# Performance work log

Hardware: AMD Instinct MI355X
Metric: run time of the kernel (lower is better)

Reference implementation:

```python
import jax, jax.numpy as jnp
import numpy as np

B, C, K, F = 16, 64, 128, 6
HORIZON_S = 3.0  # conflict_horizon_s default
EPS = 1e-06


def setup_inputs() -> dict:
    rng = np.random.default_rng(0)
    # base adjacency: sparse random directed graph, zero diagonal
    A = (rng.random((B, K, K)) < 0.05).astype(np.float32)
    A[:, np.arange(K), np.arange(K)] = 0.0
    # candidates: exactly one unordered-pair edit (state in {0:none,1:i->j,2:j->i})
    cand = np.repeat(A[:, None], C, axis=1).copy()
    i = rng.integers(0, K - 1, (B, C))
    j = i + 1 + (rng.integers(0, K - 1, (B, C)) % (K - 1 - i))
    state = rng.integers(0, 3, (B, C))
    bidx = np.arange(B)[:, None] * np.ones((1, C), dtype=np.int64)
    cidx = np.ones((B, 1), dtype=np.int64) * np.arange(C)[None, :]
    cand[bidx, cidx, i, j] = (state == 1).astype(np.float32)
    cand[bidx, cidx, j, i] = (state == 2).astype(np.float32)
    cand[:, 0] = A  # candidate 0 is NOOP (keep A_t)
    # agent features: (x, y, yaw, vx, vy, pad)
    feat = rng.normal(size=(B, K, F)).astype(np.float32)
    feat[..., 0:2] *= 20.0  # spread positions over ~40m
    mask = (rng.random((B, K)) > 0.1).astype(np.float32)
    return {
        "A_t": jnp.asarray(A),
        "candidate_A": jnp.asarray(cand),
        "agent_feat": jnp.asarray(feat),
        "agent_mask": jnp.asarray(mask),
    }


def _edit_tokens(A_t, candidate_A):
    # vectorized version of EBSTM.extract_edit_tokens
    Bn, Cn, Kn, _ = candidate_A.shape
    base = A_t > 0.5                      # [B,K,K]
    cb = candidate_A > 0.5                # [B,C,K,K]
    diff = cb != base[:, None]            # [B,C,K,K]
    upper = jnp.triu(jnp.ones((Kn, Kn), dtype=bool), k=1)
    pairdiff = (diff | jnp.swapaxes(diff, -1, -2)) & upper
    flat = pairdiff.reshape(Bn, Cn, Kn * Kn)
    changed = flat.any(-1)                # [B,C]
    idx = jnp.argmax(flat, axis=-1)       # first changed pair in row-major (i,j) order
    i = idx // Kn
    j = idx % Kn
    barange = jnp.arange(Bn)[:, None]
    carange = jnp.arange(Cn)[None, :]
    b_ij = base[barange, i, j]
    b_ji = base[barange, j, i]
    c_ij = cb[barange, carange, i, j]
    c_ji = cb[barange, carange, j, i]
    prev = jnp.where(b_ij & ~b_ji, 1, jnp.where(b_ji & ~b_ij, 2, 0))
    nxt = jnp.where(c_ij & ~c_ji, 1, jnp.where(c_ji & ~c_ij, 2, 0))
    tokens = jnp.stack([i, j, prev, nxt], axis=-1).astype(jnp.int32)
    return tokens * changed[..., None].astype(jnp.int32)


def _relation_state3(cb):
    # cb: bool [B,C,K,K]
    at = jnp.swapaxes(cb, -1, -2)
    return ((cb & ~at).astype(jnp.int32) * 1
            + (~cb & at).astype(jnp.int32) * 2
            + (cb & at).astype(jnp.int32) * 3)


def _batched_acyclic(cb, agent_mask):
    # vectorized Kahn zero-indegree peel, matching EBSTM._is_acyclic semantics:
    #  - indegree counts edges from ALL sources (valid or not)
    #  - only valid nodes are ever removed
    #  - special case: <=1 valid node is acyclic
    Bn, Cn, Kn, _ = cb.shape
    valid = (agent_mask > 0.5)[:, None, :]           # [B,1,K]
    Ai = cb.astype(jnp.int32)                        # [B,C,K,K]
    indeg = Ai.sum(axis=-2) * valid.astype(jnp.int32)  # [B,C,K]
    removed = jnp.zeros((Bn, Cn, Kn), dtype=bool)

    def body(t, carry):
        indeg, removed = carry
        rem = valid & (~removed) & (indeg == 0)
        dec = jnp.einsum('bci,bcij->bcj', rem.astype(jnp.int32), Ai)
        return indeg - dec, removed | rem

    indeg, removed = jax.lax.fori_loop(0, Kn, body, (indeg, removed))
    vcount = valid.astype(jnp.int32).sum(-1)          # [B,1]
    return (removed.astype(jnp.int32).sum(-1) == vcount) | (vcount <= 1)


def _pair_dists(agent_feat):
    pos = agent_feat[..., 0:2]
    vel = agent_feat[..., 3:5]
    # _pair_distance: d[b,i,j] = |pos_i - pos_j|
    d = jnp.linalg.norm(pos[:, :, None] - pos[:, None, :], axis=-1)
    # _pair_closest_approach_distance: r[b,i,j] = pos_j - pos_i
    r = pos[:, None, :] - pos[:, :, None]
    v = vel[:, None, :] - vel[:, :, None]
    vv = (v * v).sum(-1)
    rv = (r * v).sum(-1)
    t_star = jnp.clip(-rv / (vv + EPS), 0.0, HORIZON_S)
    dmin = jnp.linalg.norm(r + v * t_star[..., None], axis=-1)
    eye = jnp.eye(dmin.shape[-1], dtype=bool)[None]
    dmin = jnp.where(eye, jnp.inf, dmin)
    return jnp.stack([d, dmin], axis=0)  # [2,B,K,K]


def reference(A_t, candidate_A, agent_feat, agent_mask):
    cb = candidate_A > 0.5
    tokens = _edit_tokens(A_t, candidate_A)          # [B,C,4] int32
    rel = _relation_state3(cb)                       # [B,C,K,K] int32
    acyclic = _batched_acyclic(cb, agent_mask)       # [B,C] bool
    dists = _pair_dists(agent_feat)                  # [2,B,K,K] float32
    return tokens, rel, acyclic, dists
```

## Files before the change

kernel.cpp:

```cpp
#include <hip/hip_runtime.h>
#include <cstdint>
#include <math.h>

#define KN 128
#define BATCH 16
#define CAND 64

typedef float vfloat4 __attribute__((ext_vector_type(4)));

static constexpr size_t TOK_OFF = 0;
static constexpr size_t REL_OFF = (size_t)BATCH * CAND * 4;
static constexpr size_t ACY_OFF = REL_OFF + (size_t)BATCH * CAND * KN * KN;
static constexpr size_t DST_OFF = ACY_OFF + (size_t)BATCH * CAND;

#define DIAG_BIG 1.0e30f

__global__ __launch_bounds__(256) void base_bits_kernel(const float* __restrict__ A_t,
                                                        uint32_t* __restrict__ bits) {
    int tid  = blockIdx.x * 256 + threadIdx.x;
    int wave = tid >> 6;
    int lane = tid & 63;
    int half = wave & 1;
    int row  = wave >> 1;
    float v = A_t[(size_t)row * KN + half * 64 + lane];
    unsigned long long m = __ballot(v > 0.5f);
    if (lane == 0) {
        bits[row * 4 + half * 2]     = (uint32_t)m;
        bits[row * 4 + half * 2 + 1] = (uint32_t)(m >> 32);
    }
}

__global__ __launch_bounds__(256) void main_kernel(const float* __restrict__ cand,
                                                   const float* __restrict__ feat,
                                                   const float* __restrict__ mask,
                                                   const uint32_t* __restrict__ baseBits,
                                                   float* __restrict__ out) {
    __shared__ uint32_t adj[KN][5];
    __shared__ uint32_t adjW[4][KN];
    __shared__ uint32_t baseB[KN][4];
    __shared__ int      indegP[2][KN];
    __shared__ int      indeg[KN];
    __shared__ uint32_t validW[4];
    __shared__ uint32_t remW[4];
    __shared__ uint32_t removedW[4];
    __shared__ int      minIdx;

    const int t    = threadIdx.x;
    const int lane = t & 63;
    const int wave = t >> 6;
    const int bc   = blockIdx.x;
    const int b    = bc >> 6;

    const float* cptr = cand + (size_t)bc * (KN * KN);

    float4 c[16];
    const int sub = lane & 31;
    #pragma unroll
    for (int m = 0; m < 16; ++m) {
        int r = (m * 4 + wave) * 2 + (lane >> 5);
        c[m] = ((const float4*)(cptr + (size_t)r * KN))[sub];
    }

    if (t == 0) minIdx = 0x7fffffff;
    if (t < 4)  removedW[t] = 0;

    for (int w = t; w < 512; w += 256) {
        baseB[w >> 2][w & 3] = baseBits[b * 512 + w];
    }

    if (wave < 2) {
        float mv = mask[b * KN + wave * 64 + lane];
        unsigned long long m = __ballot(mv > 0.5f);
        if (lane == 0) {
            validW[wave * 2]     = (uint32_t)m;
            validW[wave * 2 + 1] = (uint32_t)(m >> 32);
        }
    }

    {
        int bi = 2 * bc + (t >> 7);
        int b2 = bi >> 7, i = bi & 127, j = t & 127;
        const float* fi = feat + (size_t)bi * 6;
        const float* fj = feat + (size_t)(b2 * KN + j) * 6;
        float pix = fi[0], piy = fi[1], vix = fi[3], viy = fi[4];
        float pjx = fj[0], pjy = fj[1], vjx = fj[3], vjy = fj[4];
        float dx = pix - pjx, dy = piy - pjy;
        float d = sqrtf(dx * dx + dy * dy);
        float rx = pjx - pix, ry = pjy - piy;
        float vx = vjx - vix, vy = vjy - viy;
        float vv = vx * vx + vy * vy;
        float rv = rx * vx + ry * vy;
        float ts = fminf(fmaxf(-rv / (vv + 1e-6f), 0.0f), 3.0f);
        float mx = rx + vx * ts, my = ry + vy * ts;
        float dmin = (i == j) ? DIAG_BIG : sqrtf(mx * mx + my * my);
        float* o = out + DST_OFF;
        __builtin_nontemporal_store(d,    o + (size_t)(b2 * KN + i) * KN + j);
        __builtin_nontemporal_store(dmin, o + (size_t)((BATCH + b2) * KN + i) * KN + j);
    }

    #pragma unroll
    for (int m = 0; m < 16; ++m) {
        int r = (m * 4 + wave) * 2 + (lane >> 5);
        const float4 v = c[m];
        uint32_t nib = (v.x > 0.5f ? 1u : 0u) | (v.y > 0.5f ? 2u : 0u) |
                       (v.z > 0.5f ? 4u : 0u) | (v.w > 0.5f ? 8u : 0u);
        uint32_t word = nib << (4 * (sub & 7));
        word |= __shfl_xor(word, 1);
        word |= __shfl_xor(word, 2);
        word |= __shfl_xor(word, 4);
        if ((lane & 7) == 0) adj[r][sub >> 3] = word;
    }
    __syncthreads();

    for (int w = t; w < 512; w += 256) {
        int iw = w >> 7, j = w & 127;
        adjW[iw][j] = adj[j][iw];
    }

    {
        int j = t & 127, half = t >> 7;
        uint32_t jw = j >> 5, jb = j & 31;
        int s = 0;
        int i0 = half * 64;
        for (int i = i0; i < i0 + 64; ++i) s += (adj[i][jw] >> jb) & 1u;
        indegP[half][j] = s;
    }

    for (int idx = t; idx < 512; idx += 256) {
        int i = idx >> 2, k = idx & 3;
        uint32_t diff = adj[i][k] ^ baseB[i][k];
        if (diff) {
            int base = k * 32;
            uint32_t up, low;
            if (i < base)            { up = diff; low = 0u; }
            else if (i >= base + 31) { up = 0u; low = (i > base + 31) ? diff : (diff & 0x7fffffffu); }
            else {
                int s = i - base;
                up  = diff & (0xffffffffu << (s + 1));
                low = diff & ((1u << s) - 1u);
            }
            int c1 = 0x7fffffff, c2 = 0x7fffffff;
            if (up)  c1 = (i << 7) | (base + __builtin_ctz(up));
            if (low) { int cc = base + __builtin_ctz(low); c2 = (cc << 7) | i; }
            int cm = min(c1, c2);
            if (cm != 0x7fffffff) atomicMin(&minIdx, cm);
        }
    }
    __syncthreads();

    if (t < KN) {
        uint32_t jw = t >> 5, jb = t & 31;
        bool valid = (validW[jw] >> jb) & 1u;
        indeg[t] = valid ? (indegP[0][t] + indegP[1][t]) : 0;
    }

    if (t == 0) {
        float* tok = out + TOK_OFF + (size_t)bc * 4;
        int mi = minIdx;
        if (mi != 0x7fffffff) {
            int i = mi >> 7, j = mi & 127;
            uint32_t b_ij = (baseB[i][j >> 5] >> (j & 31)) & 1u;
            uint32_t b_ji = (baseB[j][i >> 5] >> (i & 31)) & 1u;
            uint32_t c_ij = (adj[i][j >> 5] >> (j & 31)) & 1u;
            uint32_t c_ji = (adj[j][i >> 5] >> (i & 31)) & 1u;
            int prev = (b_ij && !b_ji) ? 1 : ((b_ji && !b_ij) ? 2 : 0);
            int nxt  = (c_ij && !c_ji) ? 1 : ((c_ji && !c_ij) ? 2 : 0);
            tok[0] = (float)i; tok[1] = (float)j; tok[2] = (float)prev; tok[3] = (float)nxt;
        } else {
            tok[0] = 0.f; tok[1] = 0.f; tok[2] = 0.f; tok[3] = 0.f;
        }
    }

    {
        float* relp = out + REL_OFF + (size_t)bc * (KN * KN);
        #pragma unroll 4
        for (int m = 0; m < 16; ++m) {
            int q  = t + 256 * m;
            int i  = q >> 5;
            int j0 = (q & 31) * 4;
            uint32_t wij = adj[i][j0 >> 5];
            int sh = j0 & 31;
            uint32_t iw = i >> 5, ib = i & 31;
            const uint4 wt = *(const uint4*)&adjW[iw][j0];
            vfloat4 o;
            o.x = (float)(((wij >> (sh + 0)) & 1u) + 2u * ((wt.x >> ib) & 1u));
            o.y = (float)(((wij >> (sh + 1)) & 1u) + 2u * ((wt.y >> ib) & 1u));
            o.z = (float)(((wij >> (sh + 2)) & 1u) + 2u * ((wt.z >> ib) & 1u));
            o.w = (float)(((wij >> (sh + 3)) & 1u) + 2u * ((wt.w >> ib) & 1u));
            __builtin_nontemporal_store(o, ((vfloat4*)relp) + q);
        }
    }
    __syncthreads();

    for (int it = 0; it < KN; ++it) {
        bool rem = false;
        if (t < KN) {
            uint32_t jw = t >> 5, jb = t & 31;
            bool valid   = (validW[jw] >> jb) & 1u;
            bool removed = (removedW[jw] >> jb) & 1u;
            rem = valid && !removed && (indeg[t] == 0);
        }
        unsigned long long m = __ballot(rem);
        if (wave < 2 && lane == 0) {
            remW[wave * 2]     = (uint32_t)m;
            remW[wave * 2 + 1] = (uint32_t)(m >> 32);
        }
        __syncthreads();
        uint32_t r0 = remW[0], r1 = remW[1], r2 = remW[2], r3 = remW[3];
        if ((r0 | r1 | r2 | r3) == 0u) break;
        if (t < 4) removedW[t] |= remW[t];
        if (t < KN) {
            uint32_t jw = t >> 5, jb = t & 31;
            int dec = 0;
            uint32_t rw[4] = {r0, r1, r2, r3};
            for (int w = 0; w < 4; ++w) {
                uint32_t mm = rw[w];
                while (mm) {
                    int i = w * 32 + __builtin_ctz(mm);
                    mm &= mm - 1;
                    dec += (adj[i][jw] >> jb) & 1u;
                }
            }
            indeg[t] -= dec;
        }
        __syncthreads();
    }
    __syncthreads();

    if (t == 0) {
        int rc = __popc(removedW[0]) + __popc(removedW[1]) + __popc(removedW[2]) + __popc(removedW[3]);
        int vc = __popc(validW[0]) + __popc(validW[1]) + __popc(validW[2]) + __popc(validW[3]);
        out[ACY_OFF + bc] = ((rc == vc) || (vc <= 1)) ? 1.0f : 0.0f;
    }
}

extern "C" void kernel_launch(void* const* d_in, const int* in_sizes, int n_in,
                              void* d_out, int out_size, void* d_ws, size_t ws_size,
                              hipStream_t stream) {
    const float* A_t  = (const float*)d_in[0];
    const float* cand = (const float*)d_in[1];
    const float* feat = (const float*)d_in[2];
    const float* mask = (const float*)d_in[3];
    float* out = (float*)d_out;
    uint32_t* bits = (uint32_t*)d_ws;

    base_bits_kernel<<<1024, 256, 0, stream>>>(A_t, bits);
    main_kernel<<<BATCH * CAND, 256, 0, stream>>>(cand, feat, mask, bits, out);
}
```

Measured before the change: 121.1 us.

## Split main kernel into prep, graph, and relation-output kernels via workspace bitmaps

Moves the pair-distance computation into the base-bits prep kernel, and takes the large relation-state output write out of the graph kernel. The graph kernel now stores packed adjacency and transpose bitmaps to workspace, and a new rel_kernel expands them into the float relation output across twice as many blocks. The aim is to keep the latency-bound topological-sort loop free of heavy store traffic and to spread the bandwidth-heavy rel write over more blocks. The cost is an extra launch plus a workspace round-trip of about 4 KB per candidate.

```diff
diff --git a/kernel.cpp b/kernel.cpp
--- a/kernel.cpp
+++ b/kernel.cpp
@@ -13,72 +13,31 @@
 static constexpr size_t ACY_OFF = REL_OFF + (size_t)BATCH * CAND * KN * KN;
 static constexpr size_t DST_OFF = ACY_OFF + (size_t)BATCH * CAND;
 
+static constexpr size_t WS_BITS = 0;
+static constexpr size_t WS_ADJ  = 8192;
+
 #define DIAG_BIG 1.0e30f
 
-__global__ __launch_bounds__(256) void base_bits_kernel(const float* __restrict__ A_t,
-                                                        uint32_t* __restrict__ bits) {
-    int tid  = blockIdx.x * 256 + threadIdx.x;
-    int wave = tid >> 6;
-    int lane = tid & 63;
-    int half = wave & 1;
-    int row  = wave >> 1;
-    float v = A_t[(size_t)row * KN + half * 64 + lane];
-    unsigned long long m = __ballot(v > 0.5f);
-    if (lane == 0) {
-        bits[row * 4 + half * 2]     = (uint32_t)m;
-        bits[row * 4 + half * 2 + 1] = (uint32_t)(m >> 32);
-    }
-}
-
-__global__ __launch_bounds__(256) void main_kernel(const float* __restrict__ cand,
+__global__ __launch_bounds__(256) void prep_kernel(const float* __restrict__ A_t,
                                                    const float* __restrict__ feat,
-                                                   const float* __restrict__ mask,
-                                                   const uint32_t* __restrict__ baseBits,
+                                                   uint32_t* __restrict__ ws,
                                                    float* __restrict__ out) {
-    __shared__ uint32_t adj[KN][5];
-    __shared__ uint32_t adjW[4][KN];
-    __shared__ uint32_t baseB[KN][4];
-    __shared__ int      indegP[2][KN];
-    __shared__ int      indeg[KN];
-    __shared__ uint32_t validW[4];
-    __shared__ uint32_t remW[4];
-    __shared__ uint32_t removedW[4];
-    __shared__ int      minIdx;
-
-    const int t    = threadIdx.x;
-    const int lane = t & 63;
-    const int wave = t >> 6;
-    const int bc   = blockIdx.x;
-    const int b    = bc >> 6;
-
-    const float* cptr = cand + (size_t)bc * (KN * KN);
-
-    float4 c[16];
-    const int sub = lane & 31;
-    #pragma unroll
-    for (int m = 0; m < 16; ++m) {
-        int r = (m * 4 + wave) * 2 + (lane >> 5);
-        c[m] = ((const float4*)(cptr + (size_t)r * KN))[sub];
-    }
-
-    if (t == 0) minIdx = 0x7fffffff;
-    if (t < 4)  removedW[t] = 0;
-
-    for (int w = t; w < 512; w += 256) {
-        baseB[w >> 2][w & 3] = baseBits[b * 512 + w];
-    }
-
-    if (wave < 2) {
-        float mv = mask[b * KN + wave * 64 + lane];
-        unsigned long long m = __ballot(mv > 0.5f);
+    int t = threadIdx.x;
+    {
+        int tid  = blockIdx.x * 256 + t;
+        int wave = tid >> 6;
+        int lane = tid & 63;
+        int half = wave & 1;
+        int row  = wave >> 1;
+        float v = A_t[(size_t)row * KN + half * 64 + lane];
+        unsigned long long m = __ballot(v > 0.5f);
         if (lane == 0) {
-            validW[wave * 2]     = (uint32_t)m;
-            validW[wave * 2 + 1] = (uint32_t)(m >> 32);
-        }
-    }
-
-    {
-        int bi = 2 * bc + (t >> 7);
+            ws[WS_BITS + row * 4 + half * 2]     = (uint32_t)m;
+            ws[WS_BITS + row * 4 + half * 2 + 1] = (uint32_t)(m >> 32);
+        }
+    }
+    {
+        int bi = 2 * blockIdx.x + (t >> 7);
         int b2 = bi >> 7, i = bi & 127, j = t & 127;
         const float* fi = feat + (size_t)bi * 6;
         const float* fj = feat + (size_t)(b2 * KN + j) * 6;
@@ -96,6 +55,53 @@
         float* o = out + DST_OFF;
         __builtin_nontemporal_store(d,    o + (size_t)(b2 * KN + i) * KN + j);
         __builtin_nontemporal_store(dmin, o + (size_t)((BATCH + b2) * KN + i) * KN + j);
+    }
+}
+
+__global__ __launch_bounds__(256) void graph_kernel(const float* __restrict__ cand,
+                                                    const float* __restrict__ mask,
+                                                    uint32_t* __restrict__ ws,
+                                                    float* __restrict__ out) {
+    __shared__ uint32_t adj[KN][5];
+    __shared__ uint32_t adjW[4][KN];
+    __shared__ uint32_t baseB[KN][4];
+    __shared__ int      indegP[2][KN];
+    __shared__ int      indeg[KN];
+    __shared__ uint32_t validW[4];
+    __shared__ uint32_t remW[4];
+    __shared__ uint32_t removedW[4];
+    __shared__ int      minIdx;
+
+    const int t    = threadIdx.x;
+    const int lane = t & 63;
+    const int wave = t >> 6;
+    const int bc   = blockIdx.x;
+    const int b    = bc >> 6;
+
+    const float* cptr = cand + (size_t)bc * (KN * KN);
+
+    float4 c[16];
+    const int sub = lane & 31;
+    #pragma unroll
+    for (int m = 0; m < 16; ++m) {
+        int r = (m * 4 + wave) * 2 + (lane >> 5);
+        c[m] = ((const float4*)(cptr + (size_t)r * KN))[sub];
+    }
+
+    if (t == 0) minIdx = 0x7fffffff;
+    if (t < 4)  removedW[t] = 0;
+
+    for (int w = t; w < 512; w += 256) {
+        baseB[w >> 2][w & 3] = ws[WS_BITS + b * 512 + w];
+    }
+
+    if (wave < 2) {
+        float mv = mask[b * KN + wave * 64 + lane];
+        unsigned long long m = __ballot(mv > 0.5f);
+        if (lane == 0) {
+            validW[wave * 2]     = (uint32_t)m;
+            validW[wave * 2 + 1] = (uint32_t)(m >> 32);
+        }
     }
 
     #pragma unroll
@@ -148,6 +154,15 @@
     }
     __syncthreads();
 
+    {
+        uint32_t* wadj = ws + WS_ADJ + (size_t)bc * 1024;
+        for (int w = t; w < 1024; w += 256) {
+            uint32_t val = (w < 512) ? adj[w >> 2][w & 3]
+                                     : adjW[(w - 512) >> 7][(w - 512) & 127];
+            __builtin_nontemporal_store(val, wadj + w);
+        }
+    }
+
     if (t < KN) {
         uint32_t jw = t >> 5, jb = t & 31;
         bool valid = (validW[jw] >> jb) & 1u;
@@ -168,26 +183,6 @@
             tok[0] = (float)i; tok[1] = (float)j; tok[2] = (float)prev; tok[3] = (float)nxt;
         } else {
             tok[0] = 0.f; tok[1] = 0.f; tok[2] = 0.f; tok[3] = 0.f;
-        }
-    }
-
-    {
-        float* relp = out + REL_OFF + (size_t)bc * (KN * KN);
-        #pragma unroll 4
-        for (int m = 0; m < 16; ++m) {
-            int q  = t + 256 * m;
-            int i  = q >> 5;
-            int j0 = (q & 31) * 4;
-            uint32_t wij = adj[i][j0 >> 5];
-            int sh = j0 & 31;
-            uint32_t iw = i >> 5, ib = i & 31;
-            const uint4 wt = *(const uint4*)&adjW[iw][j0];
-            vfloat4 o;
-            o.x = (float)(((wij >> (sh + 0)) & 1u) + 2u * ((wt.x >> ib) & 1u));
-            o.y = (float)(((wij >> (sh + 1)) & 1u) + 2u * ((wt.y >> ib) & 1u));
-            o.z = (float)(((wij >> (sh + 2)) & 1u) + 2u * ((wt.z >> ib) & 1u));
-            o.w = (float)(((wij >> (sh + 3)) & 1u) + 2u * ((wt.w >> ib) & 1u));
-            __builtin_nontemporal_store(o, ((vfloat4*)relp) + q);
         }
     }
     __syncthreads();
@@ -234,6 +229,46 @@
     }
 }
 
+__global__ __launch_bounds__(256) void rel_kernel(const uint32_t* __restrict__ ws,
+                                                  float* __restrict__ out) {
+    __shared__ uint32_t sAdj[64][4];
+    __shared__ uint32_t sAdjT[2][KN];
+
+    const int t  = threadIdx.x;
+    const int bc = blockIdx.x >> 1;
+    const int h  = blockIdx.x & 1;
+
+    const uint32_t* wadj = ws + WS_ADJ + (size_t)bc * 1024;
+
+    for (int w = t; w < 512; w += 256) {
+        if (w < 256) sAdj[w >> 2][w & 3] = wadj[(h * 64) * 4 + w];
+        else {
+            int w2 = w - 256;
+            sAdjT[w2 >> 7][w2 & 127] = wadj[512 + (2 * h) * 128 + w2];
+        }
+    }
+    __syncthreads();
+
+    float* relp = out + REL_OFF + (size_t)bc * (KN * KN);
+    #pragma unroll
+    for (int m = 0; m < 8; ++m) {
+        int q  = t + 256 * m;
+        int il = q >> 5;
+        int i  = h * 64 + il;
+        int j0 = (q & 31) * 4;
+        uint32_t wij = sAdj[il][j0 >> 5];
+        int sh = j0 & 31;
+        uint32_t ib = i & 31;
+        const uint4 wt = *(const uint4*)&sAdjT[il >> 5][j0];
+        vfloat4 o;
+        o.x = (float)(((wij >> (sh + 0)) & 1u) + 2u * ((wt.x >> ib) & 1u));
+        o.y = (float)(((wij >> (sh + 1)) & 1u) + 2u * ((wt.y >> ib) & 1u));
+        o.z = (float)(((wij >> (sh + 2)) & 1u) + 2u * ((wt.z >> ib) & 1u));
+        o.w = (float)(((wij >> (sh + 3)) & 1u) + 2u * ((wt.w >> ib) & 1u));
+        __builtin_nontemporal_store(o, ((vfloat4*)relp) + (size_t)h * 2048 + q);
+    }
+}
+
 extern "C" void kernel_launch(void* const* d_in, const int* in_sizes, int n_in,
                               void* d_out, int out_size, void* d_ws, size_t ws_size,
                               hipStream_t stream) {
@@ -242,8 +277,9 @@
     const float* feat = (const float*)d_in[2];
     const float* mask = (const float*)d_in[3];
     float* out = (float*)d_out;
-    uint32_t* bits = (uint32_t*)d_ws;
-
-    base_bits_kernel<<<1024, 256, 0, stream>>>(A_t, bits);
-    main_kernel<<<BATCH * CAND, 256, 0, stream>>>(cand, feat, mask, bits, out);
-}
+    uint32_t* ws = (uint32_t*)d_ws;
+
+    prep_kernel<<<1024, 256, 0, stream>>>(A_t, feat, ws, out);
+    graph_kernel<<<BATCH * CAND, 256, 0, stream>>>(cand, mask, ws, out);
+    rel_kernel<<<2 * BATCH * CAND, 256, 0, stream>>>(ws, out);
+}
```

New measurement: 128.1 us. +5.8%, slower.

## Transpose adjacency via ballots and use popcount-based indegree in Kahn loop

Applied to the files above, without the earlier changes.

Moves the pair-distance computation into the prep kernel alongside base-bit packing, so the main kernel only handles candidate graphs. The main kernel builds a transposed bitset with wave ballots, then uses it both for the relation-state output and for per-thread column masks. Indegrees become popcounts, and each Kahn iteration's decrement becomes a popcount of removed-mask AND column-mask instead of a per-bit loop over removed nodes. This cuts the serial work inside the topological-sort loop and one barrier, at the cost of a 64-step ballot transpose per block.

```diff
diff --git a/kernel.cpp b/kernel.cpp
--- a/kernel.cpp
+++ b/kernel.cpp
@@ -15,70 +15,26 @@
 
 #define DIAG_BIG 1.0e30f
 
-__global__ __launch_bounds__(256) void base_bits_kernel(const float* __restrict__ A_t,
-                                                        uint32_t* __restrict__ bits) {
-    int tid  = blockIdx.x * 256 + threadIdx.x;
-    int wave = tid >> 6;
-    int lane = tid & 63;
-    int half = wave & 1;
-    int row  = wave >> 1;
-    float v = A_t[(size_t)row * KN + half * 64 + lane];
-    unsigned long long m = __ballot(v > 0.5f);
-    if (lane == 0) {
-        bits[row * 4 + half * 2]     = (uint32_t)m;
-        bits[row * 4 + half * 2 + 1] = (uint32_t)(m >> 32);
-    }
-}
-
-__global__ __launch_bounds__(256) void main_kernel(const float* __restrict__ cand,
+__global__ __launch_bounds__(256) void prep_kernel(const float* __restrict__ A_t,
                                                    const float* __restrict__ feat,
-                                                   const float* __restrict__ mask,
-                                                   const uint32_t* __restrict__ baseBits,
+                                                   uint32_t* __restrict__ bits,
                                                    float* __restrict__ out) {
-    __shared__ uint32_t adj[KN][5];
-    __shared__ uint32_t adjW[4][KN];
-    __shared__ uint32_t baseB[KN][4];
-    __shared__ int      indegP[2][KN];
-    __shared__ int      indeg[KN];
-    __shared__ uint32_t validW[4];
-    __shared__ uint32_t remW[4];
-    __shared__ uint32_t removedW[4];
-    __shared__ int      minIdx;
-
-    const int t    = threadIdx.x;
-    const int lane = t & 63;
-    const int wave = t >> 6;
-    const int bc   = blockIdx.x;
-    const int b    = bc >> 6;
-
-    const float* cptr = cand + (size_t)bc * (KN * KN);
-
-    float4 c[16];
-    const int sub = lane & 31;
-    #pragma unroll
-    for (int m = 0; m < 16; ++m) {
-        int r = (m * 4 + wave) * 2 + (lane >> 5);
-        c[m] = ((const float4*)(cptr + (size_t)r * KN))[sub];
-    }
-
-    if (t == 0) minIdx = 0x7fffffff;
-    if (t < 4)  removedW[t] = 0;
-
-    for (int w = t; w < 512; w += 256) {
-        baseB[w >> 2][w & 3] = baseBits[b * 512 + w];
-    }
-
-    if (wave < 2) {
-        float mv = mask[b * KN + wave * 64 + lane];
-        unsigned long long m = __ballot(mv > 0.5f);
+    int t = threadIdx.x;
+    {
+        int tid  = blockIdx.x * 256 + t;
+        int wave = tid >> 6;
+        int lane = tid & 63;
+        int half = wave & 1;
+        int row  = wave >> 1;
+        float v = A_t[(size_t)row * KN + half * 64 + lane];
+        unsigned long long m = __ballot(v > 0.5f);
         if (lane == 0) {
-            validW[wave * 2]     = (uint32_t)m;
-            validW[wave * 2 + 1] = (uint32_t)(m >> 32);
-        }
-    }
-
-    {
-        int bi = 2 * bc + (t >> 7);
+            bits[row * 4 + half * 2]     = (uint32_t)m;
+            bits[row * 4 + half * 2 + 1] = (uint32_t)(m >> 32);
+        }
+    }
+    {
+        int bi = 2 * blockIdx.x + (t >> 7);
         int b2 = bi >> 7, i = bi & 127, j = t & 127;
         const float* fi = feat + (size_t)bi * 6;
         const float* fj = feat + (size_t)(b2 * KN + j) * 6;
@@ -97,6 +53,51 @@
         __builtin_nontemporal_store(d,    o + (size_t)(b2 * KN + i) * KN + j);
         __builtin_nontemporal_store(dmin, o + (size_t)((BATCH + b2) * KN + i) * KN + j);
     }
+}
+
+__global__ __launch_bounds__(256) void main_kernel(const float* __restrict__ cand,
+                                                   const float* __restrict__ mask,
+                                                   const uint32_t* __restrict__ baseBits,
+                                                   float* __restrict__ out) {
+    __shared__ uint32_t adj[KN][5];
+    __shared__ uint32_t adjT[KN][6];
+    __shared__ uint32_t baseB[KN][4];
+    __shared__ uint32_t validW[4];
+    __shared__ uint32_t remW[4];
+    __shared__ uint32_t removedW[4];
+    __shared__ int      minIdx;
+
+    const int t    = threadIdx.x;
+    const int lane = t & 63;
+    const int wave = t >> 6;
+    const int bc   = blockIdx.x;
+    const int b    = bc >> 6;
+
+    const float* cptr = cand + (size_t)bc * (KN * KN);
+
+    float4 c[16];
+    const int sub = lane & 31;
+    #pragma unroll
+    for (int m = 0; m < 16; ++m) {
+        int r = (m * 4 + wave) * 2 + (lane >> 5);
+        c[m] = ((const float4*)(cptr + (size_t)r * KN))[sub];
+    }
+
+    if (t == 0) minIdx = 0x7fffffff;
+    if (t < 4)  removedW[t] = 0;
+
+    for (int w = t; w < 512; w += 256) {
+        baseB[w >> 2][w & 3] = baseBits[b * 512 + w];
+    }
+
+    if (wave < 2) {
+        float mv = mask[b * KN + wave * 64 + lane];
+        unsigned long long m = __ballot(mv > 0.5f);
+        if (lane == 0) {
+            validW[wave * 2]     = (uint32_t)m;
+            validW[wave * 2 + 1] = (uint32_t)(m >> 32);
+        }
+    }
 
     #pragma unroll
     for (int m = 0; m < 16; ++m) {
@@ -112,18 +113,39 @@
     }
     __syncthreads();
 
-    for (int w = t; w < 512; w += 256) {
-        int iw = w >> 7, j = w & 127;
-        adjW[iw][j] = adj[j][iw];
-    }
-
-    {
-        int j = t & 127, half = t >> 7;
-        uint32_t jw = j >> 5, jb = j & 31;
-        int s = 0;
-        int i0 = half * 64;
-        for (int i = i0; i < i0 + 64; ++i) s += (adj[i][jw] >> jb) & 1u;
-        indegP[half][j] = s;
+    {
+        const int h = wave >> 1, q = wave & 1;
+        uint32_t rw0 = adj[h * 64 + lane][q * 2];
+        uint32_t rw1 = adj[h * 64 + lane][q * 2 + 1];
+        uint32_t myLo = 0, myHi = 0;
+        #pragma unroll
+        for (int cc = 0; cc < 64; ++cc) {
+            uint32_t w = (cc < 32) ? rw0 : rw1;
+            unsigned long long m = __ballot((w >> (cc & 31)) & 1u);
+            if (lane == cc) { myLo = (uint32_t)m; myHi = (uint32_t)(m >> 32); }
+        }
+        adjT[q * 64 + lane][2 * h]     = myLo;
+        adjT[q * 64 + lane][2 * h + 1] = myHi;
+    }
+    __syncthreads();
+
+    {
+        float* relp = out + REL_OFF + (size_t)bc * (KN * KN);
+        #pragma unroll
+        for (int m = 0; m < 16; ++m) {
+            int q  = t + 256 * m;
+            int i  = q >> 5;
+            int j0 = (q & 31) * 4;
+            int iw = j0 >> 5, sh = j0 & 31;
+            uint32_t wij = adj[i][iw];
+            uint32_t wti = adjT[i][iw];
+            vfloat4 o;
+            o.x = (float)(((wij >> (sh + 0)) & 1u) + 2u * ((wti >> (sh + 0)) & 1u));
+            o.y = (float)(((wij >> (sh + 1)) & 1u) + 2u * ((wti >> (sh + 1)) & 1u));
+            o.z = (float)(((wij >> (sh + 2)) & 1u) + 2u * ((wti >> (sh + 2)) & 1u));
+            o.w = (float)(((wij >> (sh + 3)) & 1u) + 2u * ((wti >> (sh + 3)) & 1u));
+            __builtin_nontemporal_store(o, ((vfloat4*)relp) + q);
+        }
     }
 
     for (int idx = t; idx < 512; idx += 256) {
@@ -141,18 +163,21 @@
             }
             int c1 = 0x7fffffff, c2 = 0x7fffffff;
             if (up)  c1 = (i << 7) | (base + __builtin_ctz(up));
-            if (low) { int cc = base + __builtin_ctz(low); c2 = (cc << 7) | i; }
+            if (low) { int cc2 = base + __builtin_ctz(low); c2 = (cc2 << 7) | i; }
             int cm = min(c1, c2);
             if (cm != 0x7fffffff) atomicMin(&minIdx, cm);
         }
     }
-    __syncthreads();
-
+
+    uint32_t cT0 = 0, cT1 = 0, cT2 = 0, cT3 = 0;
+    int  indeg = 0;
+    bool validT = false, removed = false;
     if (t < KN) {
-        uint32_t jw = t >> 5, jb = t & 31;
-        bool valid = (validW[jw] >> jb) & 1u;
-        indeg[t] = valid ? (indegP[0][t] + indegP[1][t]) : 0;
-    }
+        cT0 = adjT[t][0]; cT1 = adjT[t][1]; cT2 = adjT[t][2]; cT3 = adjT[t][3];
+        validT = (validW[t >> 5] >> (t & 31)) & 1u;
+        indeg = validT ? (__popc(cT0) + __popc(cT1) + __popc(cT2) + __popc(cT3)) : 0;
+    }
+    __syncthreads();
 
     if (t == 0) {
         float* tok = out + TOK_OFF + (size_t)bc * 4;
@@ -171,35 +196,8 @@
         }
     }
 
-    {
-        float* relp = out + REL_OFF + (size_t)bc * (KN * KN);
-        #pragma unroll 4
-        for (int m = 0; m < 16; ++m) {
-            int q  = t + 256 * m;
-            int i  = q >> 5;
-            int j0 = (q & 31) * 4;
-            uint32_t wij = adj[i][j0 >> 5];
-            int sh = j0 & 31;
-            uint32_t iw = i >> 5, ib = i & 31;
-            const uint4 wt = *(const uint4*)&adjW[iw][j0];
-            vfloat4 o;
-            o.x = (float)(((wij >> (sh + 0)) & 1u) + 2u * ((wt.x >> ib) & 1u));
-            o.y = (float)(((wij >> (sh + 1)) & 1u) + 2u * ((wt.y >> ib) & 1u));
-            o.z = (float)(((wij >> (sh + 2)) & 1u) + 2u * ((wt.z >> ib) & 1u));
-            o.w = (float)(((wij >> (sh + 3)) & 1u) + 2u * ((wt.w >> ib) & 1u));
-            __builtin_nontemporal_store(o, ((vfloat4*)relp) + q);
-        }
-    }
-    __syncthreads();
-
     for (int it = 0; it < KN; ++it) {
-        bool rem = false;
-        if (t < KN) {
-            uint32_t jw = t >> 5, jb = t & 31;
-            bool valid   = (validW[jw] >> jb) & 1u;
-            bool removed = (removedW[jw] >> jb) & 1u;
-            rem = valid && !removed && (indeg[t] == 0);
-        }
+        bool rem = (t < KN) && validT && !removed && (indeg == 0);
         unsigned long long m = __ballot(rem);
         if (wave < 2 && lane == 0) {
             remW[wave * 2]     = (uint32_t)m;
@@ -210,18 +208,9 @@
         if ((r0 | r1 | r2 | r3) == 0u) break;
         if (t < 4) removedW[t] |= remW[t];
         if (t < KN) {
-            uint32_t jw = t >> 5, jb = t & 31;
-            int dec = 0;
-            uint32_t rw[4] = {r0, r1, r2, r3};
-            for (int w = 0; w < 4; ++w) {
-                uint32_t mm = rw[w];
-                while (mm) {
-                    int i = w * 32 + __builtin_ctz(mm);
-                    mm &= mm - 1;
-                    dec += (adj[i][jw] >> jb) & 1u;
-                }
-            }
-            indeg[t] -= dec;
+            indeg -= __popc(r0 & cT0) + __popc(r1 & cT1) +
+                     __popc(r2 & cT2) + __popc(r3 & cT3);
+            removed = removed || rem;
         }
         __syncthreads();
     }
@@ -244,6 +233,6 @@
     float* out = (float*)d_out;
     uint32_t* bits = (uint32_t*)d_ws;
 
-    base_bits_kernel<<<1024, 256, 0, stream>>>(A_t, bits);
-    main_kernel<<<BATCH * CAND, 256, 0, stream>>>(cand, feat, mask, bits, out);
+    prep_kernel<<<1024, 256, 0, stream>>>(A_t, feat, bits, out);
+    main_kernel<<<BATCH * CAND, 256, 0, stream>>>(cand, mask, bits, out);
 }
```

New measurement: 120.8 us. About the same (-0.3%).
